# Optimization experiments

Hardware: AMD Instinct MI355X
Metric: run time of the kernel (lower is better)

Reference implementation:

```python
import jax, jax.numpy as jnp
import numpy as np

N_NODES = 50000
N_EDGES = 1600000
N_GRAPHS = 64


def setup_inputs() -> dict:
    key = jax.random.key(0)
    ks = jax.random.split(key, 16)
    p = lambda k, shape: (jax.random.normal(k, shape, dtype=jnp.float32) * 0.05)
    x = jax.random.normal(ks[0], (N_NODES, 128), dtype=jnp.float32)
    edge_index = jax.random.randint(ks[1], (2, N_EDGES), 0, N_NODES, dtype=jnp.int32)
    edge_attr = jax.random.uniform(ks[2], (N_EDGES,), dtype=jnp.float32)
    batch = jnp.sort(jax.random.randint(ks[3], (N_NODES,), 0, N_GRAPHS, dtype=jnp.int32))
    return {
        'x': x, 'edge_index': edge_index, 'edge_attr': edge_attr, 'batch': batch,
        'W1': p(ks[4], (128, 128)), 'b1': jnp.zeros((128,), jnp.float32),
        'W2': p(ks[5], (128, 64)), 'b2': jnp.zeros((64,), jnp.float32),
        'gW1': p(ks[6], (64, 32)), 'gb1': jnp.zeros((32,), jnp.float32),
        'gW2': p(ks[7], (32, 1)), 'gb2': jnp.zeros((1,), jnp.float32),
        'fcW1': p(ks[8], (64, 128)), 'fcb1': jnp.zeros((128,), jnp.float32),
        'fcW2': p(ks[9], (128, 2)), 'fcb2': jnp.zeros((2,), jnp.float32),
    }


def gcn_conv(x, src, dst, ew, W, b):
    # PyG GCNConv with edge weights: add self-loops (weight 1), symmetric norm.
    xw = x @ W  # [N, out]
    deg = jax.ops.segment_sum(ew, dst, num_segments=N_NODES) + 1.0  # self-loop
    dinv = jnp.where(deg > 0, jax.lax.rsqrt(deg), 0.0)
    coef = dinv[src] * ew * dinv[dst]  # [E]
    agg = jax.ops.segment_sum(coef[:, None] * xw[src], dst, num_segments=N_NODES)
    agg = agg + (dinv * dinv)[:, None] * xw  # self-loop contribution
    return agg + b


def global_attention(x, batch, gW1, gb1, gW2, gb2):
    # gate_nn: Linear(64,32)->ReLU->Linear(32,1), segment-softmax over graphs
    g = (jax.nn.relu(x @ gW1 + gb1) @ gW2 + gb2)[:, 0]  # [N]
    gmax = jax.ops.segment_max(g, batch, num_segments=N_GRAPHS)
    ex = jnp.exp(g - gmax[batch])
    den = jax.ops.segment_sum(ex, batch, num_segments=N_GRAPHS)
    alpha = ex / den[batch]
    return jax.ops.segment_sum(alpha[:, None] * x, batch, num_segments=N_GRAPHS)


def reference(x, edge_index, edge_attr, batch, W1, b1, W2, b2,
              gW1, gb1, gW2, gb2, fcW1, fcb1, fcW2, fcb2):
    src, dst = edge_index[0], edge_index[1]
    h = jax.nn.relu(gcn_conv(x, src, dst, edge_attr, W1, b1))
    x1 = jax.nn.relu(gcn_conv(h, src, dst, edge_attr, W2, b2))
    x2 = global_attention(x1, batch, gW1, gb1, gW2, gb2)  # [G, 64]
    # dropout is identity in eval mode
    h2 = jax.nn.relu(x2 @ fcW1 + fcb1)
    logits = h2 @ fcW2 + fcb2
    return jax.nn.log_softmax(logits, axis=1)
```

## Files before the change

kernel.cpp:

```cpp
#include <hip/hip_runtime.h>
#include <hip/hip_bf16.h>
#include <hip/hip_fp16.h>

#define N_NODES 50000
#define N_EDGES 1600000
#define N_GRAPHS 64
#define G1BLKS 1563
#define NSH 8
#define SH_STRIDE 50048
#define NBLK8 6250

__device__ __forceinline__ float coef_of(unsigned p) {
    return __half2float(__ushort_as_half((unsigned short)(p & 0xFFFFu)));
}

__global__ void mega1(const float* __restrict__ X, const float* __restrict__ W,
                      __half* __restrict__ Yh, const int* __restrict__ dst,
                      const float* __restrict__ ew,
                      unsigned long long* __restrict__ packed8,
                      unsigned short* __restrict__ pos16) {
    __shared__ float Xl[32][132];
    if (blockIdx.x >= G1BLKS) {
        const int sh = blockIdx.x & (NSH - 1);
        unsigned long long* __restrict__ pk = packed8 + (size_t)sh * SH_STRIDE;
        int e = (blockIdx.x - G1BLKS) * 256 + threadIdx.x;
        if (e < N_EDGES) {
            int d = __builtin_nontemporal_load(&dst[e]);
            float w = __builtin_nontemporal_load(&ew[e]);
            unsigned fix = (unsigned)(w * 16777216.0f);
            unsigned long long old = atomicAdd(&pk[d], 0x100000000ull | (unsigned long long)fix);
            pos16[e] = (unsigned short)((sh << 12) | (unsigned)(old >> 32));
        }
        return;
    }
    const int rt = threadIdx.x >> 5;
    const int ct = threadIdx.x & 31;
    const int base = blockIdx.x * 32;
    for (int i = threadIdx.x; i < 32 * 32; i += 256) {
        int rr = i >> 5, cc = (i & 31) << 2;
        int gr = base + rr;
        float4 v = (gr < N_NODES) ? *(const float4*)&X[(size_t)gr * 128 + cc]
                                  : make_float4(0.f, 0.f, 0.f, 0.f);
        Xl[rr][cc] = v.x; Xl[rr][cc + 1] = v.y; Xl[rr][cc + 2] = v.z; Xl[rr][cc + 3] = v.w;
    }
    __syncthreads();
    float acc[4][4] = {};
    for (int k = 0; k < 128; k += 4) {
        float4 a0 = *(const float4*)&Xl[rt * 4 + 0][k];
        float4 a1 = *(const float4*)&Xl[rt * 4 + 1][k];
        float4 a2 = *(const float4*)&Xl[rt * 4 + 2][k];
        float4 a3 = *(const float4*)&Xl[rt * 4 + 3][k];
        float4 w0 = *(const float4*)&W[(size_t)(k + 0) * 128 + ct * 4];
        float4 w1 = *(const float4*)&W[(size_t)(k + 1) * 128 + ct * 4];
        float4 w2 = *(const float4*)&W[(size_t)(k + 2) * 128 + ct * 4];
        float4 w3 = *(const float4*)&W[(size_t)(k + 3) * 128 + ct * 4];
        #define STEP(av, wv)  \
            acc[0][0] += av##0 * wv.x; acc[0][1] += av##0 * wv.y; acc[0][2] += av##0 * wv.z; acc[0][3] += av##0 * wv.w; \
            acc[1][0] += av##1 * wv.x; acc[1][1] += av##1 * wv.y; acc[1][2] += av##1 * wv.z; acc[1][3] += av##1 * wv.w; \
            acc[2][0] += av##2 * wv.x; acc[2][1] += av##2 * wv.y; acc[2][2] += av##2 * wv.z; acc[2][3] += av##2 * wv.w; \
            acc[3][0] += av##3 * wv.x; acc[3][1] += av##3 * wv.y; acc[3][2] += av##3 * wv.z; acc[3][3] += av##3 * wv.w;
        { float ax0=a0.x, ax1=a1.x, ax2=a2.x, ax3=a3.x; STEP(ax, w0) }
        { float ay0=a0.y, ay1=a1.y, ay2=a2.y, ay3=a3.y; STEP(ay, w1) }
        { float az0=a0.z, az1=a1.z, az2=a2.z, az3=a3.z; STEP(az, w2) }
        { float aw0=a0.w, aw1=a1.w, aw2=a2.w, aw3=a3.w; STEP(aw, w3) }
        #undef STEP
    }
    const int pc = ct >> 3;
    const int cw = (ct & 7) * 4;
    for (int i = 0; i < 4; ++i) {
        int gr = base + rt * 4 + i;
        if (gr < N_NODES) {
            ushort4 u;
            u.x = __half_as_ushort(__float2half(acc[i][0]));
            u.y = __half_as_ushort(__float2half(acc[i][1]));
            u.z = __half_as_ushort(__float2half(acc[i][2]));
            u.w = __half_as_ushort(__float2half(acc[i][3]));
            *(ushort4*)&Yh[((size_t)pc * N_NODES + gr) * 32 + cw] = u;
        }
    }
}

__global__ void block_sums_dinv(const unsigned long long* __restrict__ packed8,
                                int* __restrict__ bsum, float* __restrict__ dinv) {
    __shared__ int s[256];
    int idx = blockIdx.x * 256 + threadIdx.x;
    int c = 0;
    if (idx < N_NODES) {
        unsigned long long csum = 0, fsum = 0;
        #pragma unroll
        for (int sh = 0; sh < NSH; ++sh) {
            unsigned long long p = packed8[(size_t)sh * SH_STRIDE + idx];
            csum += p >> 32;
            fsum += p & 0xFFFFFFFFull;
        }
        c = (int)csum;
        dinv[idx] = rsqrtf((float)fsum * (1.0f / 16777216.0f) + 1.0f);
    }
    s[threadIdx.x] = c;
    __syncthreads();
    for (int o = 128; o; o >>= 1) {
        if (threadIdx.x < o) s[threadIdx.x] += s[threadIdx.x + o];
        __syncthreads();
    }
    if (threadIdx.x == 0) bsum[blockIdx.x] = s[0];
}

__global__ void scan_bsums(const int* __restrict__ bsum, int* __restrict__ boff,
                           int nb, int* __restrict__ row_start_last) {
    __shared__ int s[256];
    int v = (threadIdx.x < nb) ? bsum[threadIdx.x] : 0;
    s[threadIdx.x] = v;
    __syncthreads();
    for (int o = 1; o < 256; o <<= 1) {
        int t = 0;
        if (threadIdx.x >= o) t = s[threadIdx.x - o];
        __syncthreads();
        s[threadIdx.x] += t;
        __syncthreads();
    }
    if (threadIdx.x < nb) boff[threadIdx.x] = s[threadIdx.x] - v;
    if (threadIdx.x == 0) *row_start_last = N_EDGES;
}

__global__ void scan_counts(const unsigned long long* __restrict__ packed8,
                            const int* __restrict__ boff, int* __restrict__ row_start,
                            int* __restrict__ soff) {
    __shared__ int s[256];
    int idx = blockIdx.x * 256 + threadIdx.x;
    int cs[NSH];
    int v = 0;
    if (idx < N_NODES) {
        #pragma unroll
        for (int sh = 0; sh < NSH; ++sh) {
            cs[sh] = (int)(packed8[(size_t)sh * SH_STRIDE + idx] >> 32);
            v += cs[sh];
        }
    }
    s[threadIdx.x] = v;
    __syncthreads();
    for (int o = 1; o < 256; o <<= 1) {
        int t = 0;
        if (threadIdx.x >= o) t = s[threadIdx.x - o];
        __syncthreads();
        s[threadIdx.x] += t;
        __syncthreads();
    }
    if (idx < N_NODES) {
        int ex = boff[blockIdx.x] + s[threadIdx.x] - v;
        row_start[idx] = ex;
        int run = ex;
        #pragma unroll
        for (int sh = 0; sh < NSH; ++sh) {
            soff[(size_t)sh * SH_STRIDE + idx] = run;
            run += cs[sh];
        }
    }
}

__global__ void fill_direct(const int* __restrict__ src, const int* __restrict__ dst,
                            const float* __restrict__ ew, const unsigned short* __restrict__ pos16,
                            const int* __restrict__ soff, const float* __restrict__ dinv,
                            unsigned* __restrict__ csr) {
    int e = blockIdx.x * 256 + threadIdx.x;
    if (e < N_EDGES) {
        int d = __builtin_nontemporal_load(&dst[e]);
        int s = __builtin_nontemporal_load(&src[e]);
        float w = __builtin_nontemporal_load(&ew[e]);
        unsigned p16 = (unsigned)__builtin_nontemporal_load(&pos16[e]);
        int sh = (int)(p16 >> 12);
        int p  = (int)(p16 & 0xFFFu);
        float coef = dinv[s] * w * dinv[d];
        csr[soff[(size_t)sh * SH_STRIDE + d] + p] = ((unsigned)s << 16) | __half_as_ushort(__float2half(coef));
    }
}

template<int NP, bool HOUT>
__global__ void agg_csr_pair(const int* __restrict__ row_start, const unsigned* __restrict__ csr,
                             const __half* __restrict__ xwh, const float* __restrict__ dinv,
                             const float* __restrict__ b, void* __restrict__ outp) {
    constexpr int OUT = NP * 32;
    const int c    = blockIdx.x / NBLK8;
    const int nb   = blockIdx.x % NBLK8;
    const int n    = nb * 8 + (threadIdx.x >> 5);
    const int kk   = threadIdx.x & 15;
    const int half = (threadIdx.x >> 4) & 1;
    if (n >= N_NODES) return;
    const __half* __restrict__ bp = xwh + ((size_t)c * N_NODES) * 32 + 2 * kk;
    const int beg = row_start[n], end = row_start[n + 1];
    float ax = 0.f, ay = 0.f;
    int i = beg + half;
    for (; i + 6 < end; i += 8) {
        unsigned p0 = csr[i],     p1 = csr[i + 2];
        unsigned p2 = csr[i + 4], p3 = csr[i + 6];
        float2 f0 = __half22float2(*(const __half2*)(bp + (size_t)(p0 >> 16) * 32));
        float2 f1 = __half22float2(*(const __half2*)(bp + (size_t)(p1 >> 16) * 32));
        float2 f2 = __half22float2(*(const __half2*)(bp + (size_t)(p2 >> 16) * 32));
        float2 f3 = __half22float2(*(const __half2*)(bp + (size_t)(p3 >> 16) * 32));
        float e0 = coef_of(p0), e1 = coef_of(p1), e2 = coef_of(p2), e3 = coef_of(p3);
        ax += e0 * f0.x + e1 * f1.x + e2 * f2.x + e3 * f3.x;
        ay += e0 * f0.y + e1 * f1.y + e2 * f2.y + e3 * f3.y;
    }
    for (; i < end; i += 2) {
        unsigned p = csr[i];
        float2 f = __half22float2(*(const __half2*)(bp + (size_t)(p >> 16) * 32));
        float e = coef_of(p);
        ax += e * f.x; ay += e * f.y;
    }
    ax += __shfl_xor(ax, 16);
    ay += __shfl_xor(ay, 16);
    if (half == 0) {
        float2 sf = __half22float2(*(const __half2*)(bp + (size_t)n * 32));
        float dv = dinv[n];
        float dv2 = dv * dv;
        int kg = c * 32 + 2 * kk;
        float ox = fmaxf(ax + dv2 * sf.x + b[kg], 0.f);
        float oy = fmaxf(ay + dv2 * sf.y + b[kg + 1], 0.f);
        if constexpr (HOUT) {
            __half* o = (__half*)outp;
            *(__half2*)&o[(size_t)n * OUT + kg] = __floats2half2_rn(ox, oy);
        } else {
            float* o = (float*)outp;
            *(float2*)&o[(size_t)n * OUT + kg] = make_float2(ox, oy);
        }
    }
}

__global__ void gemm2_reg(const __half* __restrict__ Xh, const float* __restrict__ W,
                          __half* __restrict__ Yh, int nrows) {
    __shared__ float Xl[32][132];
    __shared__ float Wl[128][64];
    const int rt = threadIdx.x >> 5;
    const int ct = threadIdx.x & 31;
    const int base = blockIdx.x * 32;
    for (int i = threadIdx.x; i < 32 * 32; i += 256) {
        int rr = i >> 5, cc = (i & 31) << 2;
        int gr = base + rr;
        float2 fa = make_float2(0.f, 0.f), fb = fa;
        if (gr < nrows) {
            const __half2* ph = (const __half2*)&Xh[(size_t)gr * 128 + cc];
            fa = __half22float2(ph[0]);
            fb = __half22float2(ph[1]);
        }
        Xl[rr][cc] = fa.x; Xl[rr][cc + 1] = fa.y; Xl[rr][cc + 2] = fb.x; Xl[rr][cc + 3] = fb.y;
    }
    for (int i = threadIdx.x; i < 128 * 16; i += 256) {
        int kk = i >> 4, cc = (i & 15) << 2;
        *(float4*)&Wl[kk][cc] = *(const float4*)&W[(size_t)kk * 64 + cc];
    }
    float acc[4][2] = {};
    __syncthreads();
    for (int k = 0; k < 128; k += 4) {
        float4 a0 = *(const float4*)&Xl[rt * 4 + 0][k];
        float4 a1 = *(const float4*)&Xl[rt * 4 + 1][k];
        float4 a2 = *(const float4*)&Xl[rt * 4 + 2][k];
        float4 a3 = *(const float4*)&Xl[rt * 4 + 3][k];
        float2 w0 = *(const float2*)&Wl[k + 0][ct * 2];
        float2 w1 = *(const float2*)&Wl[k + 1][ct * 2];
        float2 w2 = *(const float2*)&Wl[k + 2][ct * 2];
        float2 w3 = *(const float2*)&Wl[k + 3][ct * 2];
        acc[0][0] += a0.x * w0.x; acc[0][1] += a0.x * w0.y;
        acc[1][0] += a1.x * w0.x; acc[1][1] += a1.x * w0.y;
        acc[2][0] += a2.x * w0.x; acc[2][1] += a2.x * w0.y;
        acc[3][0] += a3.x * w0.x; acc[3][1] += a3.x * w0.y;
        acc[0][0] += a0.y * w1.x; acc[0][1] += a0.y * w1.y;
        acc[1][0] += a1.y * w1.x; acc[1][1] += a1.y * w1.y;
        acc[2][0] += a2.y * w1.x; acc[2][1] += a2.y * w1.y;
        acc[3][0] += a3.y * w1.x; acc[3][1] += a3.y * w1.y;
        acc[0][0] += a0.z * w2.x; acc[0][1] += a0.z * w2.y;
        acc[1][0] += a1.z * w2.x; acc[1][1] += a1.z * w2.y;
        acc[2][0] += a2.z * w2.x; acc[2][1] += a2.z * w2.y;
        acc[3][0] += a3.z * w2.x; acc[3][1] += a3.z * w2.y;
        acc[0][0] += a0.w * w3.x; acc[0][1] += a0.w * w3.y;
        acc[1][0] += a1.w * w3.x; acc[1][1] += a1.w * w3.y;
        acc[2][0] += a2.w * w3.x; acc[2][1] += a2.w * w3.y;
        acc[3][0] += a3.w * w3.x; acc[3][1] += a3.w * w3.y;
    }
    const int col0 = ct * 2;
    const int pc   = col0 >> 5;
    const int cw   = col0 & 31;
    for (int i = 0; i < 4; ++i) {
        int gr = base + rt * 4 + i;
        if (gr < nrows) {
            __half2 hv = __floats2half2_rn(acc[i][0], acc[i][1]);
            *(__half2*)&Yh[((size_t)pc * nrows + gr) * 32 + cw] = hv;
        }
    }
}

__global__ void gate_pool(const float* __restrict__ x1, const float* __restrict__ gW1,
                          const float* __restrict__ gb1, const float* __restrict__ gW2,
                          const float* __restrict__ gb2, const int* __restrict__ batch,
                          float* __restrict__ den, float* __restrict__ pooledU) {
    __shared__ float W1l[64 * 32];
    __shared__ float W2l[32];
    __shared__ float b1l[32];
    __shared__ float el[256];
    for (int i = threadIdx.x; i < 64 * 32; i += 256) W1l[i] = gW1[i];
    if (threadIdx.x < 32) { W2l[threadIdx.x] = gW2[threadIdx.x]; b1l[threadIdx.x] = gb1[threadIdx.x]; }
    __syncthreads();
    const float gb2v = gb2[0];
    const int n0 = blockIdx.x * 256;
    const int n = n0 + threadIdx.x;
    float ev = 0.f;
    if (n < N_NODES) {
        const float* row = x1 + (size_t)n * 64;
        float t[32];
        #pragma unroll
        for (int j = 0; j < 32; ++j) t[j] = b1l[j];
        for (int k = 0; k < 64; ++k) {
            float xv = row[k];
            #pragma unroll
            for (int j = 0; j < 32; ++j) t[j] += xv * W1l[k * 32 + j];
        }
        float a = gb2v;
        #pragma unroll
        for (int j = 0; j < 32; ++j) a += fmaxf(t[j], 0.f) * W2l[j];
        ev = expf(a);
    }
    el[threadIdx.x] = ev;
    __syncthreads();
    const int f   = threadIdx.x & 63;
    const int grp = threadIdx.x >> 6;
    int start = n0 + grp * 64;
    if (start >= N_NODES) return;
    int end = min(start + 64, N_NODES);
    int cur = batch[start];
    float acc = 0.f, accd = 0.f;
    for (int m = start; m < end; ++m) {
        int bb = batch[m];
        if (bb != cur) {
            atomicAdd(&pooledU[cur * 64 + f], acc);
            if (f == 0) atomicAdd(&den[cur], accd);
            acc = 0.f; accd = 0.f; cur = bb;
        }
        float e = el[m - n0];
        acc += e * x1[(size_t)m * 64 + f];
        if (f == 0) accd += e;
    }
    atomicAdd(&pooledU[cur * 64 + f], acc);
    if (f == 0) atomicAdd(&den[cur], accd);
}

__global__ void head_kernel(const float* __restrict__ pooledU, const float* __restrict__ den,
                            const float* __restrict__ fcW1, const float* __restrict__ fcb1,
                            const float* __restrict__ fcW2, const float* __restrict__ fcb2,
                            float* __restrict__ out) {
    __shared__ float P[64];
    __shared__ float r0[2], r1[2];
    const int gi = blockIdx.x;
    if (threadIdx.x < 64) P[threadIdx.x] = pooledU[gi * 64 + threadIdx.x] / den[gi];
    __syncthreads();
    const int j = threadIdx.x;
    float a = fcb1[j];
    #pragma unroll 8
    for (int k = 0; k < 64; ++k) a += P[k] * fcW1[k * 128 + j];
    float h = fmaxf(a, 0.f);
    float p0 = h * fcW2[j * 2 + 0];
    float p1 = h * fcW2[j * 2 + 1];
    for (int o = 32; o; o >>= 1) { p0 += __shfl_xor(p0, o); p1 += __shfl_xor(p1, o); }
    if ((threadIdx.x & 63) == 0) { r0[threadIdx.x >> 6] = p0; r1[threadIdx.x >> 6] = p1; }
    __syncthreads();
    if (threadIdx.x == 0) {
        float l0 = r0[0] + r0[1] + fcb2[0];
        float l1 = r1[0] + r1[1] + fcb2[1];
        float m = fmaxf(l0, l1);
        float lse = m + logf(expf(l0 - m) + expf(l1 - m));
        out[gi * 2 + 0] = l0 - lse;
        out[gi * 2 + 1] = l1 - lse;
    }
}

extern "C" void kernel_launch(void* const* d_in, const int* in_sizes, int n_in,
                              void* d_out, int out_size, void* d_ws, size_t ws_size,
                              hipStream_t stream) {
    const float* x    = (const float*)d_in[0];
    const int*   ei   = (const int*)d_in[1];
    const float* ew   = (const float*)d_in[2];
    const int*   batch= (const int*)d_in[3];
    const float* W1   = (const float*)d_in[4];
    const float* b1   = (const float*)d_in[5];
    const float* W2   = (const float*)d_in[6];
    const float* b2   = (const float*)d_in[7];
    const float* gW1  = (const float*)d_in[8];
    const float* gb1  = (const float*)d_in[9];
    const float* gW2  = (const float*)d_in[10];
    const float* gb2  = (const float*)d_in[11];
    const float* fcW1 = (const float*)d_in[12];
    const float* fcb1 = (const float*)d_in[13];
    const float* fcW2 = (const float*)d_in[14];
    const float* fcb2 = (const float*)d_in[15];
    float* out = (float*)d_out;

    const int* src = ei;
    const int* dst = ei + N_EDGES;

    const int EB = (N_EDGES + 255) / 256;
    const int NB = (N_NODES + 255) / 256;

    float* ws = (float*)d_ws;
    __half* xwh  = (__half*)ws;
    __half* hbuf = (__half*)(ws + 3200000);
    float*  x1   = ws + 6400000;
    size_t off = 9600000;
    unsigned* csr   = (unsigned*)(ws + off); off += 1600000;
    unsigned short* pos16 = (unsigned short*)(ws + off); off += 800000;
    int*   row_start= (int*)(ws + off);    off += 50176;
    unsigned long long* packed8 = (unsigned long long*)(ws + off); off += 2 * NSH * SH_STRIDE;
    int*   soff     = (int*)(ws + off);    off += NSH * SH_STRIDE;
    float* dinv     = ws + off;            off += 50176;
    int*   bsum     = (int*)(ws + off);    off += 256;
    int*   boff     = (int*)(ws + off);    off += 256;
    float* den      = ws + off;            off += 64;
    float* pooled   = ws + off;            off += 4096;

    hipMemsetAsync(packed8, 0, (size_t)NSH * SH_STRIDE * sizeof(unsigned long long), stream);
    hipMemsetAsync(den, 0, (64 + 4096) * sizeof(float), stream);

    mega1<<<G1BLKS + EB, 256, 0, stream>>>(x, W1, xwh, dst, ew, packed8, pos16);

    block_sums_dinv<<<NB, 256, 0, stream>>>(packed8, bsum, dinv);
    scan_bsums<<<1, 256, 0, stream>>>(bsum, boff, NB, row_start + N_NODES);
    scan_counts<<<NB, 256, 0, stream>>>(packed8, boff, row_start, soff);
    fill_direct<<<EB, 256, 0, stream>>>(src, dst, ew, pos16, soff, dinv, csr);

    agg_csr_pair<4, true><<<4 * NBLK8, 256, 0, stream>>>(row_start, csr, xwh, dinv, b1, hbuf);

    gemm2_reg<<<(N_NODES + 31) / 32, 256, 0, stream>>>(hbuf, W2, xwh, N_NODES);
    agg_csr_pair<2, false><<<2 * NBLK8, 256, 0, stream>>>(row_start, csr, xwh, dinv, b2, x1);

    gate_pool<<<NB, 256, 0, stream>>>(x1, gW1, gb1, gW2, gb2, batch, den, pooled);

    head_kernel<<<N_GRAPHS, 128, 0, stream>>>(pooled, den, fcW1, fcb1, fcW2, fcb2, out);
}
```

Baseline: 308.4 us.

## Prefetch CSR entries in aggregation, store x1 in fp16, stage in LDS for gate_pool

The aggregation loop now software-pipelines its CSR index loads, fetching the next group of four packed entries while the current gathers are in flight. The second GCN layer output is written as fp16 instead of fp32, which halves that intermediate's traffic. gate_pool stages each block's 256x64 tile of x1 into shared memory and reuses it for both the gate MLP and the pooling pass, replacing strided per-thread global reads. This costs about 66KB of LDS per gate_pool block, which lowers its occupancy, and adds fp16 rounding to x1.

```diff
diff --git a/kernel.cpp b/kernel.cpp
--- a/kernel.cpp
+++ b/kernel.cpp
@@ -189,16 +189,23 @@
     const int beg = row_start[n], end = row_start[n + 1];
     float ax = 0.f, ay = 0.f;
     int i = beg + half;
-    for (; i + 6 < end; i += 8) {
-        unsigned p0 = csr[i],     p1 = csr[i + 2];
-        unsigned p2 = csr[i + 4], p3 = csr[i + 6];
-        float2 f0 = __half22float2(*(const __half2*)(bp + (size_t)(p0 >> 16) * 32));
-        float2 f1 = __half22float2(*(const __half2*)(bp + (size_t)(p1 >> 16) * 32));
-        float2 f2 = __half22float2(*(const __half2*)(bp + (size_t)(p2 >> 16) * 32));
-        float2 f3 = __half22float2(*(const __half2*)(bp + (size_t)(p3 >> 16) * 32));
-        float e0 = coef_of(p0), e1 = coef_of(p1), e2 = coef_of(p2), e3 = coef_of(p3);
+    unsigned c0 = 0, c1 = 0, c2 = 0, c3 = 0;
+    if (i + 6 < end) { c0 = csr[i]; c1 = csr[i + 2]; c2 = csr[i + 4]; c3 = csr[i + 6]; }
+    while (i + 6 < end) {
+        __half2 h0 = *(const __half2*)(bp + (size_t)(c0 >> 16) * 32);
+        __half2 h1 = *(const __half2*)(bp + (size_t)(c1 >> 16) * 32);
+        __half2 h2 = *(const __half2*)(bp + (size_t)(c2 >> 16) * 32);
+        __half2 h3 = *(const __half2*)(bp + (size_t)(c3 >> 16) * 32);
+        float e0 = coef_of(c0), e1 = coef_of(c1), e2 = coef_of(c2), e3 = coef_of(c3);
+        int ni = i + 8;
+        unsigned d0 = 0, d1 = 0, d2 = 0, d3 = 0;
+        if (ni + 6 < end) { d0 = csr[ni]; d1 = csr[ni + 2]; d2 = csr[ni + 4]; d3 = csr[ni + 6]; }
+        float2 f0 = __half22float2(h0), f1 = __half22float2(h1);
+        float2 f2 = __half22float2(h2), f3 = __half22float2(h3);
         ax += e0 * f0.x + e1 * f1.x + e2 * f2.x + e3 * f3.x;
         ay += e0 * f0.y + e1 * f1.y + e2 * f2.y + e3 * f3.y;
+        c0 = d0; c1 = d1; c2 = d2; c3 = d3;
+        i = ni;
     }
     for (; i < end; i += 2) {
         unsigned p = csr[i];
@@ -287,28 +294,42 @@
     }
 }
 
-__global__ void gate_pool(const float* __restrict__ x1, const float* __restrict__ gW1,
+__global__ void gate_pool(const __half* __restrict__ x1h, const float* __restrict__ gW1,
                           const float* __restrict__ gb1, const float* __restrict__ gW2,
                           const float* __restrict__ gb2, const int* __restrict__ batch,
                           float* __restrict__ den, float* __restrict__ pooledU) {
     __shared__ float W1l[64 * 32];
     __shared__ float W2l[32];
     __shared__ float b1l[32];
+    __shared__ float Xs[256][65];
     __shared__ float el[256];
     for (int i = threadIdx.x; i < 64 * 32; i += 256) W1l[i] = gW1[i];
     if (threadIdx.x < 32) { W2l[threadIdx.x] = gW2[threadIdx.x]; b1l[threadIdx.x] = gb1[threadIdx.x]; }
+    const int n0 = blockIdx.x * 256;
+    for (int i = threadIdx.x; i < 256 * 16; i += 256) {
+        int r = i >> 4, c4 = (i & 15) << 2;
+        int nn = n0 + r;
+        if (nn < N_NODES) {
+            ushort4 u = *(const ushort4*)&x1h[(size_t)nn * 64 + c4];
+            Xs[r][c4 + 0] = __half2float(__ushort_as_half(u.x));
+            Xs[r][c4 + 1] = __half2float(__ushort_as_half(u.y));
+            Xs[r][c4 + 2] = __half2float(__ushort_as_half(u.z));
+            Xs[r][c4 + 3] = __half2float(__ushort_as_half(u.w));
+        } else {
+            Xs[r][c4 + 0] = 0.f; Xs[r][c4 + 1] = 0.f;
+            Xs[r][c4 + 2] = 0.f; Xs[r][c4 + 3] = 0.f;
+        }
+    }
     __syncthreads();
     const float gb2v = gb2[0];
-    const int n0 = blockIdx.x * 256;
     const int n = n0 + threadIdx.x;
     float ev = 0.f;
     if (n < N_NODES) {
-        const float* row = x1 + (size_t)n * 64;
         float t[32];
         #pragma unroll
         for (int j = 0; j < 32; ++j) t[j] = b1l[j];
         for (int k = 0; k < 64; ++k) {
-            float xv = row[k];
+            float xv = Xs[threadIdx.x][k];
             #pragma unroll
             for (int j = 0; j < 32; ++j) t[j] += xv * W1l[k * 32 + j];
         }
@@ -334,7 +355,7 @@
             acc = 0.f; accd = 0.f; cur = bb;
         }
         float e = el[m - n0];
-        acc += e * x1[(size_t)m * 64 + f];
+        acc += e * Xs[m - n0][f];
         if (f == 0) accd += e;
     }
     atomicAdd(&pooledU[cur * 64 + f], acc);
@@ -400,7 +421,7 @@
     float* ws = (float*)d_ws;
     __half* xwh  = (__half*)ws;
     __half* hbuf = (__half*)(ws + 3200000);
-    float*  x1   = ws + 6400000;
+    __half* x1h  = (__half*)(ws + 6400000);
     size_t off = 9600000;
     unsigned* csr   = (unsigned*)(ws + off); off += 1600000;
     unsigned short* pos16 = (unsigned short*)(ws + off); off += 800000;
@@ -426,9 +447,9 @@
     agg_csr_pair<4, true><<<4 * NBLK8, 256, 0, stream>>>(row_start, csr, xwh, dinv, b1, hbuf);
 
     gemm2_reg<<<(N_NODES + 31) / 32, 256, 0, stream>>>(hbuf, W2, xwh, N_NODES);
-    agg_csr_pair<2, false><<<2 * NBLK8, 256, 0, stream>>>(row_start, csr, xwh, dinv, b2, x1);
-
-    gate_pool<<<NB, 256, 0, stream>>>(x1, gW1, gb1, gW2, gb2, batch, den, pooled);
+    agg_csr_pair<2, true><<<2 * NBLK8, 256, 0, stream>>>(row_start, csr, xwh, dinv, b2, x1h);
+
+    gate_pool<<<NB, 256, 0, stream>>>(x1h, gW1, gb1, gW2, gb2, batch, den, pooled);
 
     head_kernel<<<N_GRAPHS, 128, 0, stream>>>(pooled, den, fcW1, fcb1, fcW2, fcb2, out);
 }
```

Result: faster. 298.1 us (-3.4%).
